# Performance work log

Hardware: AMD Instinct MI355X
Metric: run time of the kernel (lower is better)

The kernel has to match this reference:

```python
import jax, jax.numpy as jnp
import numpy as np


def setup_inputs() -> dict:
    key = jax.random.key(0)
    N, L, S, H, E = 2, 2048, 2048, 8, 64
    k0, k1, k2, k3 = jax.random.split(key, 4)
    queries = jax.random.normal(k0, (N, L, H, E), dtype=jnp.float32)
    keys = jax.random.normal(k1, (N, S, H, E), dtype=jnp.float32)
    values = jax.random.normal(k2, (N, S, H, E), dtype=jnp.float32)
    Erel = jax.random.normal(k3, (L, E), dtype=jnp.float32)  # self.E relative embedding table
    # causal additive mask: 0 where key <= query, -1e9 elsewhere
    attn_mask_add = jnp.where(jnp.arange(S)[None, :] <= jnp.arange(L)[:, None], 0.0, -1e9).astype(jnp.float32)
    key_len_add = jnp.zeros((N, S), dtype=jnp.float32)  # full-length sequences
    return {"queries": queries, "keys": keys, "values": values, "Erel": Erel,
            "attn_mask_add": attn_mask_add, "key_len_add": key_len_add}


def reference(queries, keys, values, Erel, attn_mask_add, key_len_add):
    N, L, H, E = queries.shape
    S = keys.shape[1]
    temp = 1.0 / np.sqrt(E)
    q = (queries * temp).transpose(0, 2, 1, 3)   # [N,H,L,E]
    k = keys.transpose(0, 2, 1, 3)               # [N,H,S,E]
    # relative logits: QE [N,H,L,M], M = L (E table has L rows)
    QE = jnp.einsum('nhle,me->nhlm', q, Erel)
    M = QE.shape[-1]
    # _qe_masking: keep qe[i, j] where j >= M - 1 - i
    i = jnp.arange(L)[:, None]
    j = jnp.arange(M)[None, :]
    QE = QE * (j >= (M - 1 - i)).astype(QE.dtype)
    # _skewing: pad one zero column on the left, reshape swapping last two dims, drop first row
    padded = jnp.pad(QE, ((0, 0), (0, 0), (0, 0), (1, 0)))          # [N,H,L,M+1]
    Srel = padded.reshape(N, H, M + 1, L)[:, :, 1:, :]               # [N,H,M,L] == [N,H,L,S] since M==L==S
    QK = (jnp.einsum('nhle,nhse->nhls', q, k)
          + Srel
          + attn_mask_add[None, None, :, :]
          + key_len_add[:, None, None, :])
    A = jax.nn.softmax(QK, axis=-1)  # dropout disabled (eval-mode reference)
    V = jnp.einsum('nhls,nshd->nlhd', A, values)
    return V
```

## Files before the change

### kernel.cpp

```cpp
#include <hip/hip_runtime.h>
#include <hip/hip_bf16.h>


typedef __attribute__((ext_vector_type(8))) short bf16x8;
typedef __attribute__((ext_vector_type(4))) float f32x4;
typedef unsigned short u16;

#define L_Q 2048
#define S_K 2048
#define N_H 8
#define E_D 64
#define RSTRIDE 512
#define LOG2E 1.44269504088896f

#define QW_OFF 0u
#define KW_OFF (4u << 20)
#define VT_OFF (8u << 20)
#define EW_OFF (12u << 20)
#define ML_OFF ((12u << 20) + (512u << 10))
#define OW_OFF ((13u << 20) + (512u << 10))
#define WS_PACK ((size_t)ML_OFF)
#define WS_FULL ((size_t)OW_OFF + (size_t)2048 * 4096 * 2)

static __device__ __forceinline__ short f2bf(float f) {
  unsigned u = __builtin_bit_cast(unsigned, f);
  u += 0x7fffu + ((u >> 16) & 1u);
  return (short)(u >> 16);
}

static __device__ __forceinline__ float bf2f(u16 u) {
  return __builtin_bit_cast(float, ((unsigned)u) << 16);
}

static __device__ __forceinline__ unsigned pk2(float a, float b) {
  return (unsigned)(u16)f2bf(a) | ((unsigned)(u16)f2bf(b) << 16);
}

static __device__ __forceinline__ bf16x8 loadpack8(const float* __restrict__ p, float scale) {
  float4 a = *reinterpret_cast<const float4*>(p);
  float4 b = *reinterpret_cast<const float4*>(p + 4);
  bf16x8 r;
  r[0] = f2bf(a.x * scale); r[1] = f2bf(a.y * scale);
  r[2] = f2bf(a.z * scale); r[3] = f2bf(a.w * scale);
  r[4] = f2bf(b.x * scale); r[5] = f2bf(b.y * scale);
  r[6] = f2bf(b.z * scale); r[7] = f2bf(b.w * scale);
  return r;
}

__global__ __launch_bounds__(256)
void pack_qke(const float* __restrict__ Qf, const float* __restrict__ Kf,
              const float* __restrict__ Ef, u16* __restrict__ Qw,
              u16* __restrict__ Kw, u16* __restrict__ Ew) {
  const unsigned u = blockIdx.x * 256 + threadIdx.x;
  if (u < 1048576u) {
    const unsigned v  = u & 524287u;
    const int e  = (v & 15) * 4;
    const int i  = (v >> 4) & 2047;
    const int nh = v >> 15;
    const int n = nh >> 3, h = nh & 7;
    const size_t src = ((size_t)(n * L_Q + i) * N_H + h) * E_D + e;
    const size_t dst = ((size_t)nh * L_Q + i) * E_D + e;
    const bool isQ = u < 524288u;
    float4 x = *reinterpret_cast<const float4*>((isQ ? Qf : Kf) + src);
    const float s = isQ ? 0.125f * LOG2E : 1.0f;
    ushort4 o;
    o.x = (u16)f2bf(x.x * s); o.y = (u16)f2bf(x.y * s);
    o.z = (u16)f2bf(x.z * s); o.w = (u16)f2bf(x.w * s);
    *reinterpret_cast<ushort4*>((isQ ? Qw : Kw) + dst) = o;
  } else {
    const unsigned v = u - 1048576u;
    if (v < 32768u) {
      const size_t idx = (size_t)v * 4;
      float4 x = *reinterpret_cast<const float4*>(Ef + idx);
      ushort4 o;
      o.x = (u16)f2bf(x.x); o.y = (u16)f2bf(x.y);
      o.z = (u16)f2bf(x.z); o.w = (u16)f2bf(x.w);
      *reinterpret_cast<ushort4*>(Ew + idx) = o;
    }
  }
}

__global__ __launch_bounds__(256)
void pack_vt(const float* __restrict__ Vf, u16* __restrict__ Vtw) {
  __shared__ u16 t[64][72];
  const int j0 = blockIdx.x * 64;
  const int nh = blockIdx.y;
  const int n = nh >> 3, h = nh & 7;
  const int tid = threadIdx.x;
  {
    const int jr = tid >> 2, dg = (tid & 3) * 16;
    const float* src = Vf + ((size_t)(n * L_Q + j0 + jr) * N_H + h) * E_D + dg;
#pragma unroll
    for (int q = 0; q < 4; ++q) {
      float4 x = *reinterpret_cast<const float4*>(src + q * 4);
      t[jr][dg + q * 4 + 0] = (u16)f2bf(x.x);
      t[jr][dg + q * 4 + 1] = (u16)f2bf(x.y);
      t[jr][dg + q * 4 + 2] = (u16)f2bf(x.z);
      t[jr][dg + q * 4 + 3] = (u16)f2bf(x.w);
    }
  }
  __syncthreads();
  {
    const int dr = tid >> 2, jg = (tid & 3) * 16;
    u16 tmp[16];
#pragma unroll
    for (int jj = 0; jj < 16; ++jj) tmp[jj] = t[jg + jj][dr];
    u16* dst = Vtw + ((size_t)nh * E_D + dr) * S_K + j0 + jg;
    *reinterpret_cast<uint4*>(dst)     = *reinterpret_cast<uint4*>(&tmp[0]);
    *reinterpret_cast<uint4*>(dst + 8) = *reinterpret_cast<uint4*>(&tmp[8]);
  }
}

template <bool SPLIT>
__global__ __launch_bounds__(256, 3)
void relattn_r14(const u16* __restrict__ Qw, const u16* __restrict__ Kw,
                 const u16* __restrict__ Vtw, const u16* __restrict__ Ew,
                 const float* __restrict__ KLp, float* __restrict__ Op,
                 u16* __restrict__ OwP, float* __restrict__ MLp) {
  const int bid = blockIdx.x;
  const int nh = bid & 15;
  const int n = nh >> 3, h = nh & 7;
  const int rest = bid >> 4;
  const int wq64 = SPLIT ? (31 - (rest >> 2))
                         : ((rest < 16) ? (31 - rest) : (rest - 16));
  const int sp = SPLIT ? (rest & 3) : 0;
  const int iw64 = wq64 * 64;
  const int tid = threadIdx.x;
  const int wid = tid >> 6;
  const int lane = tid & 63;
  const int lo = lane & 15, hi = lane >> 4;
  const int iw = iw64 + wid * 16;
  const int nt = wq64 + 1;
  const int t0 = SPLIT ? ((sp * nt) >> 2) : 0;
  const int t1 = SPLIT ? (((sp + 1) * nt) >> 2) : nt;
  const int s = (wq64 * 16 + nh) * 4 + sp;

  __shared__ u16 Kls[2][64 * 64];
  __shared__ u16 Vls[2][64 * 64];
  __shared__ float qe_lds[4][16 * 80];

  if (SPLIT && t0 >= t1) {
    u16* OwH = OwP + (size_t)s * 4096 + wid * 1024 + lane * 4;
    ushort4 z4 = {0, 0, 0, 0};
#pragma unroll
    for (int dt = 0; dt < 4; ++dt)
      *reinterpret_cast<ushort4*>(OwH + dt * 256) = z4;
    if (lane < 16) {
      MLp[s * 128 + wid * 32 + lane] = -1e30f;
      MLp[s * 128 + wid * 32 + 16 + lane] = 0.f;
    }
    return;
  }

  const u16* Kg = Kw + (size_t)nh * S_K * E_D;
  const u16* Vg = Vtw + (size_t)nh * E_D * S_K;
  const float* klq = KLp + (size_t)n * S_K + 4 * hi;
  const u16* epl = Ew + (size_t)(2032 - iw) * E_D + lo * E_D + hi * 8;

  const int srow = lane >> 3;
  const int scc  = lane & 7;
  const int r0 = wid * 8 + srow;
  const int r1 = r0 + 32;
  const int swc = (scc ^ srow) * 8;
  uint4 stK[2], stV[2];

  auto LOAD_KV = [&](int jj0) {
    stK[0] = *reinterpret_cast<const uint4*>(Kg + (size_t)(jj0 + r0) * E_D + scc * 8);
    stK[1] = *reinterpret_cast<const uint4*>(Kg + (size_t)(jj0 + r1) * E_D + scc * 8);
    stV[0] = *reinterpret_cast<const uint4*>(Vg + (size_t)r0 * S_K + jj0 + scc * 8);
    stV[1] = *reinterpret_cast<const uint4*>(Vg + (size_t)r1 * S_K + jj0 + scc * 8);
  };
  auto WRITE_KV = [&](int bb) {
    *reinterpret_cast<uint4*>(&Kls[bb][r0 * 64 + swc]) = stK[0];
    *reinterpret_cast<uint4*>(&Kls[bb][r1 * 64 + swc]) = stK[1];
    *reinterpret_cast<uint4*>(&Vls[bb][r0 * 64 + swc]) = stV[0];
    *reinterpret_cast<uint4*>(&Vls[bb][r1 * 64 + swc]) = stV[1];
  };

  bf16x8 efc[8];
  auto LOAD_EFC = [&](int tt64) {
#pragma unroll
    for (int kt = 0; kt < 2; ++kt)
#pragma unroll
      for (int tt = 1; tt < 5; ++tt)
        efc[kt * 4 + tt - 1] = *reinterpret_cast<const bf16x8*>(
            epl + (size_t)(tt64 * 64 + tt * 16) * E_D + kt * 32);
  };

  bf16x8 qa[2];
  {
    const u16* qrow = Qw + ((size_t)nh * L_Q + iw + lo) * E_D + hi * 8;
    qa[0] = *reinterpret_cast<const bf16x8*>(qrow);
    qa[1] = *reinterpret_cast<const bf16x8*>(qrow + 32);
  }

  LOAD_KV(t0 * 64);
  WRITE_KV(0);
  if (t0 + 1 < t1) LOAD_KV((t0 + 1) * 64);
  LOAD_EFC(t0);
  __syncthreads();

  f32x4 o_acc[4] = {};
  float m_run = -1e30f, l_run = 0.f;
  const float* rb = &qe_lds[wid][lo * 80 + (15 - lo) + 4 * hi];
  const int lsw = lo & 7;
  int b = 0;
  f32x4 qe_carry = {};

  for (int t = t0; t < t1; ++t) {
    const int j0 = t * 64;
    if (t + 1 < t1) WRITE_KV(b ^ 1);
    if (t + 2 < t1) LOAD_KV(j0 + 128);

    __builtin_amdgcn_s_setprio(1);
    f32x4 s_acc[4] = {};
#pragma unroll
    for (int kt = 0; kt < 2; ++kt)
#pragma unroll
      for (int ct = 0; ct < 4; ++ct) {
        const bf16x8 kf = *reinterpret_cast<const bf16x8*>(
            &Kls[b][(ct * 16 + lo) * 64 + (((kt * 4 + hi) ^ lsw) * 8)]);
        s_acc[ct] = __builtin_amdgcn_mfma_f32_16x16x32_bf16(kf, qa[kt], s_acc[ct], 0, 0, 0);
      }

    f32x4 qe_acc[5];
    if (t == t0) {
      f32x4 z = {};
      qe_acc[0] = z;
#pragma unroll
      for (int kt = 0; kt < 2; ++kt) {
        const bf16x8 e0 = *reinterpret_cast<const bf16x8*>(
            epl + (size_t)(t0 * 64) * E_D + kt * 32);
        qe_acc[0] = __builtin_amdgcn_mfma_f32_16x16x32_bf16(e0, qa[kt], qe_acc[0], 0, 0, 0);
      }
    } else {
      qe_acc[0] = qe_carry;
    }
#pragma unroll
    for (int tt = 1; tt < 5; ++tt) { f32x4 z = {}; qe_acc[tt] = z; }
#pragma unroll
    for (int kt = 0; kt < 2; ++kt)
#pragma unroll
      for (int tt = 1; tt < 5; ++tt)
        qe_acc[tt] = __builtin_amdgcn_mfma_f32_16x16x32_bf16(efc[kt * 4 + tt - 1], qa[kt],
                                                             qe_acc[tt], 0, 0, 0);
    qe_carry = qe_acc[4];
    __builtin_amdgcn_s_setprio(0);

    if (t + 1 < t1) LOAD_EFC(t + 1);

#pragma unroll
    for (int tt = 0; tt < 5; ++tt)
      *reinterpret_cast<f32x4*>(&qe_lds[wid][lo * 80 + tt * 16 + 4 * hi]) = qe_acc[tt];

    float4 klv[4];
#pragma unroll
    for (int ct = 0; ct < 4; ++ct)
      klv[ct] = *reinterpret_cast<const float4*>(klq + j0 + ct * 16);

    const bool maskt = (t == nt - 1);
    const int thr = iw + lo - j0 - 4 * hi;
    float p[4][4];
#pragma unroll
    for (int ct = 0; ct < 4; ++ct) {
      const float k0 = klv[ct].x * LOG2E, k1 = klv[ct].y * LOG2E;
      const float k2 = klv[ct].z * LOG2E, k3 = klv[ct].w * LOG2E;
      p[ct][0] = s_acc[ct][0] + rb[ct * 16 + 0] + k0;
      p[ct][1] = s_acc[ct][1] + rb[ct * 16 + 1] + k1;
      p[ct][2] = s_acc[ct][2] + rb[ct * 16 + 2] + k2;
      p[ct][3] = s_acc[ct][3] + rb[ct * 16 + 3] + k3;
      if (maskt) {
#pragma unroll
        for (int g = 0; g < 4; ++g)
          if (ct * 16 + g > thr) p[ct][g] = -1e30f;
      }
    }

    float a0 = fmaxf(fmaxf(p[0][0], p[0][1]), fmaxf(p[0][2], p[0][3]));
    float a1 = fmaxf(fmaxf(p[1][0], p[1][1]), fmaxf(p[1][2], p[1][3]));
    float a2 = fmaxf(fmaxf(p[2][0], p[2][1]), fmaxf(p[2][2], p[2][3]));
    float a3 = fmaxf(fmaxf(p[3][0], p[3][1]), fmaxf(p[3][2], p[3][3]));
    float tmax = fmaxf(fmaxf(a0, a1), fmaxf(a2, a3));
    tmax = fmaxf(tmax, __shfl_xor(tmax, 16));
    tmax = fmaxf(tmax, __shfl_xor(tmax, 32));
    const float mnew = fmaxf(m_run, tmax);
    const float alpha = exp2f(m_run - mnew);
#pragma unroll
    for (int ct = 0; ct < 4; ++ct)
#pragma unroll
      for (int g = 0; g < 4; ++g)
        p[ct][g] = exp2f(p[ct][g] - mnew);
    float s0 = (p[0][0] + p[0][1]) + (p[0][2] + p[0][3]);
    float s1 = (p[1][0] + p[1][1]) + (p[1][2] + p[1][3]);
    float s2 = (p[2][0] + p[2][1]) + (p[2][2] + p[2][3]);
    float s3 = (p[3][0] + p[3][1]) + (p[3][2] + p[3][3]);
    float rs = (s0 + s1) + (s2 + s3);
    rs += __shfl_xor(rs, 16);
    rs += __shfl_xor(rs, 32);
    l_run = l_run * alpha + rs;
    m_run = mnew;

#pragma unroll
    for (int dt = 0; dt < 4; ++dt) o_acc[dt] = o_acc[dt] * alpha;

    uint4 w0, w1;
    w0.x = pk2(p[0][0], p[0][1]); w0.y = pk2(p[0][2], p[0][3]);
    w0.z = pk2(p[1][0], p[1][1]); w0.w = pk2(p[1][2], p[1][3]);
    w1.x = pk2(p[2][0], p[2][1]); w1.y = pk2(p[2][2], p[2][3]);
    w1.z = pk2(p[3][0], p[3][1]); w1.w = pk2(p[3][2], p[3][3]);
    const bf16x8 pb0 = __builtin_bit_cast(bf16x8, w0);
    const bf16x8 pb1 = __builtin_bit_cast(bf16x8, w1);

    __builtin_amdgcn_s_setprio(1);
#pragma unroll
    for (int kt = 0; kt < 2; ++kt)
#pragma unroll
      for (int dt = 0; dt < 4; ++dt) {
        const int vrow = dt * 16 + lo;
        const int ch = kt * 4 + (hi >> 1);
        const uint2 va2 = *reinterpret_cast<const uint2*>(
            &Vls[b][vrow * 64 + ((ch ^ lsw) * 8) + (hi & 1) * 4]);
        const uint2 vb2 = *reinterpret_cast<const uint2*>(
            &Vls[b][vrow * 64 + (((ch + 2) ^ lsw) * 8) + (hi & 1) * 4]);
        uint4 uw; uw.x = va2.x; uw.y = va2.y; uw.z = vb2.x; uw.w = vb2.y;
        const bf16x8 vf = __builtin_bit_cast(bf16x8, uw);
        o_acc[dt] = __builtin_amdgcn_mfma_f32_16x16x32_bf16(vf, kt ? pb1 : pb0, o_acc[dt], 0, 0, 0);
      }
    __builtin_amdgcn_s_setprio(0);

    __syncthreads();
    b ^= 1;
  }

  if (SPLIT) {
    u16* OwH = OwP + (size_t)s * 4096 + wid * 1024 + lane * 4;
#pragma unroll
    for (int dt = 0; dt < 4; ++dt) {
      ushort4 o4;
      o4.x = (u16)f2bf(o_acc[dt][0]); o4.y = (u16)f2bf(o_acc[dt][1]);
      o4.z = (u16)f2bf(o_acc[dt][2]); o4.w = (u16)f2bf(o_acc[dt][3]);
      *reinterpret_cast<ushort4*>(OwH + dt * 256) = o4;
    }
    if (lane < 16) {
      MLp[s * 128 + wid * 32 + lane] = m_run;
      MLp[s * 128 + wid * 32 + 16 + lane] = l_run;
    }
  } else {
    const float inv = 1.f / l_run;
    float* ob = Op + (size_t)n * L_Q * RSTRIDE + h * E_D + (size_t)(iw + lo) * RSTRIDE;
#pragma unroll
    for (int dt = 0; dt < 4; ++dt) {
      f32x4 o = o_acc[dt] * inv;
      *reinterpret_cast<f32x4*>(ob + dt * 16 + 4 * hi) = o;
    }
  }
}

__global__ __launch_bounds__(256)
void combine4(const u16* __restrict__ Owh, const float* __restrict__ MLp,
              float* __restrict__ Op) {
  const int pair = blockIdx.x;
  const int nh = pair & 15;
  const int wq64 = pair >> 4;
  const int n = nh >> 3, h = nh & 7;
  const int tid = threadIdx.x;
  const int wid = tid >> 6;
  const int lane = tid & 63;
  const int lo = lane & 15, hi = lane >> 4;
  const int sb = pair * 4;

  float m[4], l[4];
#pragma unroll
  for (int i = 0; i < 4; ++i) {
    m[i] = MLp[(sb + i) * 128 + wid * 32 + lo];
    l[i] = MLp[(sb + i) * 128 + wid * 32 + 16 + lo];
  }
  float M = fmaxf(fmaxf(m[0], m[1]), fmaxf(m[2], m[3]));
  float w[4]; float den = 0.f;
#pragma unroll
  for (int i = 0; i < 4; ++i) { w[i] = exp2f(m[i] - M); den += l[i] * w[i]; }
  const float inv = 1.f / den;

  float* ob = Op + (size_t)n * L_Q * RSTRIDE + h * E_D
            + (size_t)(wq64 * 64 + wid * 16 + lo) * RSTRIDE;
#pragma unroll
  for (int dt = 0; dt < 4; ++dt) {
    f32x4 acc = {};
#pragma unroll
    for (int i = 0; i < 4; ++i) {
      const ushort4 v = *reinterpret_cast<const ushort4*>(
          Owh + (size_t)(sb + i) * 4096 + wid * 1024 + dt * 256 + lane * 4);
      acc[0] += w[i] * bf2f(v.x);
      acc[1] += w[i] * bf2f(v.y);
      acc[2] += w[i] * bf2f(v.z);
      acc[3] += w[i] * bf2f(v.w);
    }
    f32x4 o = acc * inv;
    *reinterpret_cast<f32x4*>(ob + dt * 16 + 4 * hi) = o;
  }
}

__global__ __launch_bounds__(64, 2)
void relattn_fb(const float* __restrict__ Qf, const float* __restrict__ Kf,
                const float* __restrict__ Vf, const float* __restrict__ Ef,
                const float* __restrict__ KLp, float* __restrict__ Op) {
  const int bid = blockIdx.x;
  const int nh = bid & 15;
  const int n = nh >> 3, h = nh & 7;
  const int wq = 127 - (bid >> 4);
  const int iw = wq * 16;
  const int lane = threadIdx.x & 63;
  const int lo = lane & 15, hi = lane >> 4;

  __shared__ u16 p_lds[16 * 72];

  const float* klp = KLp + (size_t)n * S_K;
  float* ob = Op + (size_t)n * L_Q * RSTRIDE + h * E_D;

  bf16x8 qa[2];
  const float* qb = Qf + ((size_t)(n * L_Q + iw + lo) * N_H + h) * E_D + hi * 8;
  qa[0] = loadpack8(qb, 0.125f);
  qa[1] = loadpack8(qb + 32, 0.125f);

  f32x4 o_acc[4] = {};
  float m_run[4], l_run[4];
#pragma unroll
  for (int g = 0; g < 4; ++g) { m_run[g] = -1e30f; l_run[g] = 0.f; }

  const int ntiles = (wq >> 2) + 1;
  for (int t = 0; t < ntiles; ++t) {
    const int j0 = t * 64;
    f32x4 s_acc[4] = {};
#pragma unroll
    for (int kt = 0; kt < 2; ++kt)
#pragma unroll
      for (int ct = 0; ct < 4; ++ct) {
        bf16x8 kf = loadpack8(Kf + ((size_t)(n * S_K + j0 + ct * 16 + lo) * N_H + h) * E_D
                                  + kt * 32 + hi * 8, 1.f);
        s_acc[ct] = __builtin_amdgcn_mfma_f32_16x16x32_bf16(qa[kt], kf, s_acc[ct], 0, 0, 0);
      }
    const int mbase = (L_Q - 1) - (iw + 15) + j0;
    f32x4 qe_acc[5] = {};
#pragma unroll
    for (int kt = 0; kt < 2; ++kt)
#pragma unroll
      for (int tt = 0; tt < 5; ++tt) {
        int mr = mbase + tt * 16 + lo;
        mr = mr > (L_Q - 1) ? (L_Q - 1) : mr;
        bf16x8 ef = loadpack8(Ef + (size_t)mr * E_D + kt * 32 + hi * 8, 1.f);
        qe_acc[tt] = __builtin_amdgcn_mfma_f32_16x16x32_bf16(qa[kt], ef, qe_acc[tt], 0, 0, 0);
      }
    float kladd[4];
#pragma unroll
    for (int ct = 0; ct < 4; ++ct) kladd[ct] = klp[j0 + ct * 16 + lo];
    float sv[4][4];
#pragma unroll
    for (int ct = 0; ct < 4; ++ct) {
      const int jj = ct * 16 + lo;
#pragma unroll
      for (int g = 0; g < 4; ++g) {
        const int r = 4 * hi + g;
        const int u = jj - r + 15;
        const int srcl = (u & 15) | (hi << 4);
        const float a = __shfl(qe_acc[ct][g], srcl);
        const float bq = __shfl(qe_acc[ct + 1][g], srcl);
        const float rel = (lo <= r) ? a : bq;
        float sv2 = s_acc[ct][g] + rel + kladd[ct];
        if (j0 + jj > iw + r) sv2 = -1e9f;
        sv[ct][g] = sv2;
      }
    }
    float alpha[4];
#pragma unroll
    for (int g = 0; g < 4; ++g) {
      float mx = fmaxf(fmaxf(sv[0][g], sv[1][g]), fmaxf(sv[2][g], sv[3][g]));
      mx = fmaxf(mx, __shfl_xor(mx, 1));
      mx = fmaxf(mx, __shfl_xor(mx, 2));
      mx = fmaxf(mx, __shfl_xor(mx, 4));
      mx = fmaxf(mx, __shfl_xor(mx, 8));
      const float mnew = fmaxf(m_run[g], mx);
      const float al = __expf(m_run[g] - mnew);
      float rsv = 0.f;
#pragma unroll
      for (int ct = 0; ct < 4; ++ct) {
        const float pv = __expf(sv[ct][g] - mnew);
        sv[ct][g] = pv;
        rsv += pv;
      }
      rsv += __shfl_xor(rsv, 1);
      rsv += __shfl_xor(rsv, 2);
      rsv += __shfl_xor(rsv, 4);
      rsv += __shfl_xor(rsv, 8);
      l_run[g] = l_run[g] * al + rsv;
      m_run[g] = mnew;
      alpha[g] = al;
    }
#pragma unroll
    for (int dt = 0; dt < 4; ++dt)
#pragma unroll
      for (int g = 0; g < 4; ++g)
        o_acc[dt][g] *= alpha[g];
#pragma unroll
    for (int ct = 0; ct < 4; ++ct)
#pragma unroll
      for (int g = 0; g < 4; ++g)
        p_lds[(4 * hi + g) * 72 + ct * 16 + lo] = (u16)f2bf(sv[ct][g]);
#pragma unroll
    for (int jt = 0; jt < 2; ++jt) {
      const bf16x8 pav = *reinterpret_cast<const bf16x8*>(&p_lds[lo * 72 + jt * 32 + hi * 8]);
#pragma unroll
      for (int dt = 0; dt < 4; ++dt) {
        bf16x8 vf;
        const float* vp = Vf + ((size_t)(n * S_K + j0 + jt * 32 + hi * 8) * N_H + h) * E_D
                            + dt * 16 + lo;
#pragma unroll
        for (int e = 0; e < 8; ++e) vf[e] = f2bf(vp[(size_t)e * RSTRIDE]);
        o_acc[dt] = __builtin_amdgcn_mfma_f32_16x16x32_bf16(pav, vf, o_acc[dt], 0, 0, 0);
      }
    }
  }
  float inv[4];
#pragma unroll
  for (int g = 0; g < 4; ++g) inv[g] = 1.f / l_run[g];
#pragma unroll
  for (int dt = 0; dt < 4; ++dt)
#pragma unroll
    for (int g = 0; g < 4; ++g)
      ob[(size_t)(iw + 4 * hi + g) * RSTRIDE + dt * 16 + lo] = o_acc[dt][g] * inv[g];
}

extern "C" void kernel_launch(void* const* d_in, const int* in_sizes, int n_in,
                              void* d_out, int out_size, void* d_ws, size_t ws_size,
                              hipStream_t stream) {
  const float* Q  = (const float*)d_in[0];
  const float* K  = (const float*)d_in[1];
  const float* V  = (const float*)d_in[2];
  const float* E  = (const float*)d_in[3];
  const float* KL = (const float*)d_in[5];
  float* O = (float*)d_out;

  char* ws = (char*)d_ws;
  u16* Qw   = (u16*)(ws + QW_OFF);
  u16* Kw   = (u16*)(ws + KW_OFF);
  u16* Vtw  = (u16*)(ws + VT_OFF);
  u16* Ew   = (u16*)(ws + EW_OFF);
  float* ML = (float*)(ws + ML_OFF);
  u16* Ow   = (u16*)(ws + OW_OFF);

  const bool ws_pack = ws_size >= WS_PACK;
  const bool ws_full = ws_size >= WS_FULL;

  if (ws_pack) {
    hipLaunchKernelGGL(pack_qke, dim3((1048576 + 32768 + 255) / 256), dim3(256), 0, stream,
                       Q, K, E, Qw, Kw, Ew);
    hipLaunchKernelGGL(pack_vt, dim3(32, 16), dim3(256), 0, stream, V, Vtw);
  }
  if (ws_full) {
    hipLaunchKernelGGL((relattn_r14<true>), dim3(2048), dim3(256), 0, stream,
                       Qw, Kw, Vtw, Ew, KL, O, Ow, ML);
    hipLaunchKernelGGL(combine4, dim3(512), dim3(256), 0, stream, Ow, ML, O);
  } else if (ws_pack) {
    hipLaunchKernelGGL((relattn_r14<false>), dim3(512), dim3(256), 0, stream,
                       Qw, Kw, Vtw, Ew, KL, O, Ow, ML);
  } else {
    hipLaunchKernelGGL(relattn_fb, dim3(2048), dim3(64), 0, stream, Q, K, V, E, KL, O);
  }
}
```

Before: 94.20 us.

## Widen attention query tile to 128 rows with 8 waves per block

Each workgroup now handles 128 query rows with 8 wavefronts instead of 64 rows with 4. Every K/V tile staged in LDS is therefore shared by twice as many query rows, halving global K/V traffic, and each thread loads one row instead of two. The masking condition becomes a per-wave diagonal test, since the last tile is no longer the only masked one. The grid and combine kernel are resized and partial-output strides doubled to match. The trade-off is fewer, larger blocks, more causal-diagonal waste in the final tiles, and a launch bound of 4 blocks of 512 threads that may raise register pressure.

```diff
diff --git a/kernel.cpp b/kernel.cpp
--- a/kernel.cpp
+++ b/kernel.cpp
@@ -20,7 +20,7 @@
 #define ML_OFF ((12u << 20) + (512u << 10))
 #define OW_OFF ((13u << 20) + (512u << 10))
 #define WS_PACK ((size_t)ML_OFF)
-#define WS_FULL ((size_t)OW_OFF + (size_t)2048 * 4096 * 2)
+#define WS_FULL ((size_t)OW_OFF + (size_t)1024 * 8192 * 2)
 
 static __device__ __forceinline__ short f2bf(float f) {
   unsigned u = __builtin_bit_cast(unsigned, f);
@@ -112,8 +112,8 @@
 }
 
 template <bool SPLIT>
-__global__ __launch_bounds__(256, 3)
-void relattn_r14(const u16* __restrict__ Qw, const u16* __restrict__ Kw,
+__global__ __launch_bounds__(512, 4)
+void relattn_r17(const u16* __restrict__ Qw, const u16* __restrict__ Kw,
                  const u16* __restrict__ Vtw, const u16* __restrict__ Ew,
                  const float* __restrict__ KLp, float* __restrict__ Op,
                  u16* __restrict__ OwP, float* __restrict__ MLp) {
@@ -121,33 +121,33 @@
   const int nh = bid & 15;
   const int n = nh >> 3, h = nh & 7;
   const int rest = bid >> 4;
-  const int wq64 = SPLIT ? (31 - (rest >> 2))
-                         : ((rest < 16) ? (31 - rest) : (rest - 16));
+  const int wq128 = SPLIT ? (15 - (rest >> 2))
+                          : ((rest < 8) ? (15 - rest) : (rest - 8));
   const int sp = SPLIT ? (rest & 3) : 0;
-  const int iw64 = wq64 * 64;
+  const int iw128 = wq128 * 128;
   const int tid = threadIdx.x;
   const int wid = tid >> 6;
   const int lane = tid & 63;
   const int lo = lane & 15, hi = lane >> 4;
-  const int iw = iw64 + wid * 16;
-  const int nt = wq64 + 1;
+  const int iw = iw128 + wid * 16;
+  const int nt = 2 * wq128 + 2;
   const int t0 = SPLIT ? ((sp * nt) >> 2) : 0;
   const int t1 = SPLIT ? (((sp + 1) * nt) >> 2) : nt;
-  const int s = (wq64 * 16 + nh) * 4 + sp;
+  const int s = (wq128 * 16 + nh) * 4 + sp;
 
   __shared__ u16 Kls[2][64 * 64];
   __shared__ u16 Vls[2][64 * 64];
-  __shared__ float qe_lds[4][16 * 80];
+  __shared__ float qe_lds[8][16 * 80];
 
   if (SPLIT && t0 >= t1) {
-    u16* OwH = OwP + (size_t)s * 4096 + wid * 1024 + lane * 4;
+    u16* OwH = OwP + (size_t)s * 8192 + wid * 1024 + lane * 4;
     ushort4 z4 = {0, 0, 0, 0};
 #pragma unroll
     for (int dt = 0; dt < 4; ++dt)
       *reinterpret_cast<ushort4*>(OwH + dt * 256) = z4;
     if (lane < 16) {
-      MLp[s * 128 + wid * 32 + lane] = -1e30f;
-      MLp[s * 128 + wid * 32 + 16 + lane] = 0.f;
+      MLp[s * 256 + wid * 32 + lane] = -1e30f;
+      MLp[s * 256 + wid * 32 + 16 + lane] = 0.f;
     }
     return;
   }
@@ -159,22 +159,17 @@
 
   const int srow = lane >> 3;
   const int scc  = lane & 7;
-  const int r0 = wid * 8 + srow;
-  const int r1 = r0 + 32;
+  const int r = wid * 8 + srow;
   const int swc = (scc ^ srow) * 8;
-  uint4 stK[2], stV[2];
+  uint4 stK, stV;
 
   auto LOAD_KV = [&](int jj0) {
-    stK[0] = *reinterpret_cast<const uint4*>(Kg + (size_t)(jj0 + r0) * E_D + scc * 8);
-    stK[1] = *reinterpret_cast<const uint4*>(Kg + (size_t)(jj0 + r1) * E_D + scc * 8);
-    stV[0] = *reinterpret_cast<const uint4*>(Vg + (size_t)r0 * S_K + jj0 + scc * 8);
-    stV[1] = *reinterpret_cast<const uint4*>(Vg + (size_t)r1 * S_K + jj0 + scc * 8);
+    stK = *reinterpret_cast<const uint4*>(Kg + (size_t)(jj0 + r) * E_D + scc * 8);
+    stV = *reinterpret_cast<const uint4*>(Vg + (size_t)r * S_K + jj0 + scc * 8);
   };
   auto WRITE_KV = [&](int bb) {
-    *reinterpret_cast<uint4*>(&Kls[bb][r0 * 64 + swc]) = stK[0];
-    *reinterpret_cast<uint4*>(&Kls[bb][r1 * 64 + swc]) = stK[1];
-    *reinterpret_cast<uint4*>(&Vls[bb][r0 * 64 + swc]) = stV[0];
-    *reinterpret_cast<uint4*>(&Vls[bb][r1 * 64 + swc]) = stV[1];
+    *reinterpret_cast<uint4*>(&Kls[bb][r * 64 + swc]) = stK;
+    *reinterpret_cast<uint4*>(&Vls[bb][r * 64 + swc]) = stV;
   };
 
   bf16x8 efc[8];
@@ -258,7 +253,7 @@
     for (int ct = 0; ct < 4; ++ct)
       klv[ct] = *reinterpret_cast<const float4*>(klq + j0 + ct * 16);
 
-    const bool maskt = (t == nt - 1);
+    const bool maskt = (j0 + 63 > iw);
     const int thr = iw + lo - j0 - 4 * hi;
     float p[4][4];
 #pragma unroll
@@ -333,7 +328,7 @@
   }
 
   if (SPLIT) {
-    u16* OwH = OwP + (size_t)s * 4096 + wid * 1024 + lane * 4;
+    u16* OwH = OwP + (size_t)s * 8192 + wid * 1024 + lane * 4;
 #pragma unroll
     for (int dt = 0; dt < 4; ++dt) {
       ushort4 o4;
@@ -342,8 +337,8 @@
       *reinterpret_cast<ushort4*>(OwH + dt * 256) = o4;
     }
     if (lane < 16) {
-      MLp[s * 128 + wid * 32 + lane] = m_run;
-      MLp[s * 128 + wid * 32 + 16 + lane] = l_run;
+      MLp[s * 256 + wid * 32 + lane] = m_run;
+      MLp[s * 256 + wid * 32 + 16 + lane] = l_run;
     }
   } else {
     const float inv = 1.f / l_run;
@@ -356,12 +351,12 @@
   }
 }
 
-__global__ __launch_bounds__(256)
+__global__ __launch_bounds__(512)
 void combine4(const u16* __restrict__ Owh, const float* __restrict__ MLp,
               float* __restrict__ Op) {
   const int pair = blockIdx.x;
   const int nh = pair & 15;
-  const int wq64 = pair >> 4;
+  const int wq128 = pair >> 4;
   const int n = nh >> 3, h = nh & 7;
   const int tid = threadIdx.x;
   const int wid = tid >> 6;
@@ -372,8 +367,8 @@
   float m[4], l[4];
 #pragma unroll
   for (int i = 0; i < 4; ++i) {
-    m[i] = MLp[(sb + i) * 128 + wid * 32 + lo];
-    l[i] = MLp[(sb + i) * 128 + wid * 32 + 16 + lo];
+    m[i] = MLp[(sb + i) * 256 + wid * 32 + lo];
+    l[i] = MLp[(sb + i) * 256 + wid * 32 + 16 + lo];
   }
   float M = fmaxf(fmaxf(m[0], m[1]), fmaxf(m[2], m[3]));
   float w[4]; float den = 0.f;
@@ -382,14 +377,14 @@
   const float inv = 1.f / den;
 
   float* ob = Op + (size_t)n * L_Q * RSTRIDE + h * E_D
-            + (size_t)(wq64 * 64 + wid * 16 + lo) * RSTRIDE;
+            + (size_t)(wq128 * 128 + wid * 16 + lo) * RSTRIDE;
 #pragma unroll
   for (int dt = 0; dt < 4; ++dt) {
     f32x4 acc = {};
 #pragma unroll
     for (int i = 0; i < 4; ++i) {
       const ushort4 v = *reinterpret_cast<const ushort4*>(
-          Owh + (size_t)(sb + i) * 4096 + wid * 1024 + dt * 256 + lane * 4);
+          Owh + (size_t)(sb + i) * 8192 + wid * 1024 + dt * 256 + lane * 4);
       acc[0] += w[i] * bf2f(v.x);
       acc[1] += w[i] * bf2f(v.y);
       acc[2] += w[i] * bf2f(v.z);
@@ -459,14 +454,14 @@
       const int jj = ct * 16 + lo;
 #pragma unroll
       for (int g = 0; g < 4; ++g) {
-        const int r = 4 * hi + g;
-        const int u = jj - r + 15;
+        const int rr = 4 * hi + g;
+        const int u = jj - rr + 15;
         const int srcl = (u & 15) | (hi << 4);
         const float a = __shfl(qe_acc[ct][g], srcl);
         const float bq = __shfl(qe_acc[ct + 1][g], srcl);
-        const float rel = (lo <= r) ? a : bq;
+        const float rel = (lo <= rr) ? a : bq;
         float sv2 = s_acc[ct][g] + rel + kladd[ct];
-        if (j0 + jj > iw + r) sv2 = -1e9f;
+        if (j0 + jj > iw + rr) sv2 = -1e9f;
         sv[ct][g] = sv2;
       }
     }
@@ -556,11 +551,11 @@
     hipLaunchKernelGGL(pack_vt, dim3(32, 16), dim3(256), 0, stream, V, Vtw);
   }
   if (ws_full) {
-    hipLaunchKernelGGL((relattn_r14<true>), dim3(2048), dim3(256), 0, stream,
+    hipLaunchKernelGGL((relattn_r17<true>), dim3(1024), dim3(512), 0, stream,
                        Qw, Kw, Vtw, Ew, KL, O, Ow, ML);
-    hipLaunchKernelGGL(combine4, dim3(512), dim3(256), 0, stream, Ow, ML, O);
+    hipLaunchKernelGGL(combine4, dim3(256), dim3(512), 0, stream, Ow, ML, O);
   } else if (ws_pack) {
-    hipLaunchKernelGGL((relattn_r14<false>), dim3(512), dim3(256), 0, stream,
+    hipLaunchKernelGGL((relattn_r17<false>), dim3(256), dim3(512), 0, stream,
                        Qw, Kw, Vtw, Ew, KL, O, Ow, ML);
   } else {
     hipLaunchKernelGGL(relattn_fb, dim3(2048), dim3(64), 0, stream, Q, K, V, E, KL, O);
```

Result: faster. 85.73 us (-9.0%).
